# Optimization experiments

Measured on AMD Instinct MI355X. Metric: run time of the kernel, lower is better.

The kernel has to match this reference:

```python
import jax, jax.numpy as jnp
import numpy as np

N, D = 65536, 2000


def setup_inputs() -> dict:
    key = jax.random.key(0)
    factor = jax.random.normal(key, (N, D), dtype=jnp.float32)
    weight = jnp.float32(0.01)
    return {"factor": factor, "weight": weight}


def reference(factor, weight):
    # trace(factor[1:] @ factor[:-1].T) == sum of row-wise dot products of
    # shifted rows; O(n*d) instead of the original's O(n^2*d) matmul.
    n = factor.shape[0]
    tr = jnp.sum(factor[1:] * factor[:-1])
    return -weight * tr / (n - 1)
```

## Files before the change

### kernel.cpp

```cpp
#include <hip/hip_runtime.h>


#define N_ROWS 65536
#define D_COLS 2000
#define NBLOCKS 1024
#define NTHREADS 512
#define ROWS_PER_BLOCK 64

__global__ __launch_bounds__(NTHREADS) void shifted_dot_colwise(
    const float* __restrict__ a,
    const float* __restrict__ weight,
    float* __restrict__ out) {
    const int t = threadIdx.x;

    float4 acc = make_float4(0.f, 0.f, 0.f, 0.f);

    if (t < D_COLS / 4) {
        const int r0 = blockIdx.x * ROWS_PER_BLOCK;
        int r1 = r0 + ROWS_PER_BLOCK;
        if (r1 > N_ROWS - 1) r1 = N_ROWS - 1;

        const float4* col = (const float4*)(a + (long long)r0 * D_COLS) + t;
        const int row4 = D_COLS / 4;

        float4 prev = col[0];
        #pragma unroll 4
        for (int n = r0 + 1; n <= r1; ++n) {
            col += row4;
            float4 curr = *col;
            acc.x += prev.x * curr.x;
            acc.y += prev.y * curr.y;
            acc.z += prev.z * curr.z;
            acc.w += prev.w * curr.w;
            prev = curr;
        }
    }

    float s = acc.x + acc.y + acc.z + acc.w;

    #pragma unroll
    for (int off = 32; off > 0; off >>= 1)
        s += __shfl_down(s, off, 64);

    __shared__ float wave_sums[NTHREADS / 64];
    int lane = t & 63;
    int wid  = t >> 6;
    if (lane == 0) wave_sums[wid] = s;
    __syncthreads();

    if (t == 0) {
        float tot = 0.f;
        #pragma unroll
        for (int i = 0; i < NTHREADS / 64; ++i) tot += wave_sums[i];
        float w = weight[0];
        atomicAdd(out, tot * (-w / (float)(N_ROWS - 1)));
    }
}

extern "C" void kernel_launch(void* const* d_in, const int* in_sizes, int n_in,
                              void* d_out, int out_size, void* d_ws, size_t ws_size,
                              hipStream_t stream) {
    const float* factor = (const float*)d_in[0];
    const float* weight = (const float*)d_in[1];
    float* out = (float*)d_out;

    hipMemsetAsync(out, 0, sizeof(float), stream);

    dim3 grid(NBLOCKS), block(NTHREADS);
    shifted_dot_colwise<<<grid, block, 0, stream>>>(factor, weight, out);
}
```

Before: 665.1 us.

## Stream whole rows per wavefront over contiguous row bands

Each wavefront now owns a contiguous band of 16 rows and reads every full row itself, 8 float4 per lane with a masked tail, keeping the previous row in registers. Previously a block of 512 threads split one row by column, leaving 12 threads idle, and only 1024 blocks ran. The new layout gives each wave more loads in flight and avoids idle threads. In exchange it uses more registers for the row buffers, which may lower occupancy, and halves the block count.

```diff
diff --git a/kernel.cpp b/kernel.cpp
--- a/kernel.cpp
+++ b/kernel.cpp
@@ -1,38 +1,60 @@
 #include <hip/hip_runtime.h>
 
 
-#define N_ROWS 65536
-#define D_COLS 2000
-#define NBLOCKS 1024
+#define N_ROWS   65536
+#define D_COLS   2000
+#define ROW4     (D_COLS / 4)
 #define NTHREADS 512
-#define ROWS_PER_BLOCK 64
+#define NBLOCKS  512
+#define WPB      (NTHREADS / 64)
+#define NWAVES   (NBLOCKS * WPB)
+#define BAND     (N_ROWS / NWAVES)
 
-__global__ __launch_bounds__(NTHREADS) void shifted_dot_colwise(
+__global__ __launch_bounds__(NTHREADS) void shifted_dot_wavestream(
     const float* __restrict__ a,
     const float* __restrict__ weight,
     float* __restrict__ out) {
-    const int t = threadIdx.x;
+    const int lane = threadIdx.x & 63;
+    const int wid  = threadIdx.x >> 6;
+    const int w    = blockIdx.x * WPB + wid;
+
+    const long long r0 = (long long)w * BAND;
+    long long r1 = r0 + BAND;
+    if (r1 > N_ROWS - 1) r1 = N_ROWS - 1;
+
+    const float4* row = (const float4*)a + r0 * ROW4;
+    const bool tail = (lane < 52);
+
+    float4 prev[8];
+    #pragma unroll
+    for (int p = 0; p < 7; ++p) prev[p] = row[p * 64 + lane];
+    if (tail) prev[7] = row[448 + lane];
 
     float4 acc = make_float4(0.f, 0.f, 0.f, 0.f);
 
-    if (t < D_COLS / 4) {
-        const int r0 = blockIdx.x * ROWS_PER_BLOCK;
-        int r1 = r0 + ROWS_PER_BLOCK;
-        if (r1 > N_ROWS - 1) r1 = N_ROWS - 1;
+    #pragma unroll 2
+    for (long long n = r0; n < r1; ++n) {
+        row += ROW4;
+        float4 c[7];
+        #pragma unroll
+        for (int p = 0; p < 7; ++p) c[p] = row[p * 64 + lane];
+        float4 c7;
+        if (tail) c7 = row[448 + lane];
 
-        const float4* col = (const float4*)(a + (long long)r0 * D_COLS) + t;
-        const int row4 = D_COLS / 4;
-
-        float4 prev = col[0];
-        #pragma unroll 4
-        for (int n = r0 + 1; n <= r1; ++n) {
-            col += row4;
-            float4 curr = *col;
-            acc.x += prev.x * curr.x;
-            acc.y += prev.y * curr.y;
-            acc.z += prev.z * curr.z;
-            acc.w += prev.w * curr.w;
-            prev = curr;
+        #pragma unroll
+        for (int p = 0; p < 7; ++p) {
+            acc.x += prev[p].x * c[p].x;
+            acc.y += prev[p].y * c[p].y;
+            acc.z += prev[p].z * c[p].z;
+            acc.w += prev[p].w * c[p].w;
+            prev[p] = c[p];
+        }
+        if (tail) {
+            acc.x += prev[7].x * c7.x;
+            acc.y += prev[7].y * c7.y;
+            acc.z += prev[7].z * c7.z;
+            acc.w += prev[7].w * c7.w;
+            prev[7] = c7;
         }
     }
 
@@ -42,18 +64,16 @@
     for (int off = 32; off > 0; off >>= 1)
         s += __shfl_down(s, off, 64);
 
-    __shared__ float wave_sums[NTHREADS / 64];
-    int lane = t & 63;
-    int wid  = t >> 6;
+    __shared__ float wave_sums[WPB];
     if (lane == 0) wave_sums[wid] = s;
     __syncthreads();
 
-    if (t == 0) {
+    if (threadIdx.x == 0) {
         float tot = 0.f;
         #pragma unroll
-        for (int i = 0; i < NTHREADS / 64; ++i) tot += wave_sums[i];
-        float w = weight[0];
-        atomicAdd(out, tot * (-w / (float)(N_ROWS - 1)));
+        for (int i = 0; i < WPB; ++i) tot += wave_sums[i];
+        float wgt = weight[0];
+        atomicAdd(out, tot * (-wgt / (float)(N_ROWS - 1)));
     }
 }
 
@@ -67,5 +87,5 @@
     hipMemsetAsync(out, 0, sizeof(float), stream);
 
     dim3 grid(NBLOCKS), block(NTHREADS);
-    shifted_dot_colwise<<<grid, block, 0, stream>>>(factor, weight, out);
+    shifted_dot_wavestream<<<grid, block, 0, stream>>>(factor, weight, out);
 }
```

Measured after the change: 667.0 us. No clear change (+0.3%).
